# Optimization experiments

Hardware: AMD Instinct MI355X
Metric: run time of the kernel (lower is better)

Reference implementation:

```python
import jax, jax.numpy as jnp
import numpy as np

B, H, W, D = 16, 64, 64, 512

def setup_inputs() -> dict:
    key = jax.random.key(0)
    k1, k2, k3, k4, k5, k6 = jax.random.split(key, 6)
    x = jax.random.normal(k1, (B, H, W, D), dtype=jnp.float32)
    attentionXFull = jax.random.normal(k2, (B, H, W, W), dtype=jnp.float32)
    attentionYFull = jax.random.normal(k3, (B, W, H, H), dtype=jnp.float32)
    valueFull = jax.random.normal(k4, (B, H, W, D), dtype=jnp.float32)
    # Learned scalar Gaussian params: shift initialized positive, bias negative
    shift = jnp.abs(jax.random.normal(k5, (1,), dtype=jnp.float32))
    bias = -jnp.abs(jax.random.normal(k6, (1,), dtype=jnp.float32))
    return {"x": x, "attentionXFull": attentionXFull, "attentionYFull": attentionYFull,
            "valueFull": valueFull, "shift": shift, "bias": bias}

def reference(x, attentionXFull, attentionYFull, valueFull, shift, bias):
    # valueFull: [B,H,W,D]; attentionXFull: [B,H,W,W] (last axis = row positions h)
    # attentionYFull: [B,W,H,H] (indexed [b,c,r,w], last axis = col positions w)
    Bv, Hd, Wd, Dd = valueFull.shape
    cw = jnp.arange(Wd, dtype=valueFull.dtype)
    # disX[c,h] = -(shift*(h-c)^2 + bias)
    disX = -(shift[0] * (cw[None, :] - cw[:, None]) ** 2 + bias[0])  # [W,W]
    aX = jax.nn.sigmoid(disX[None, None, :, :] + attentionXFull)     # [B,H,W,W]
    outX = jnp.einsum('brch,brhd->brcd', aX, valueFull)              # row attention
    rh = jnp.arange(Hd, dtype=valueFull.dtype)
    # disY[r,w] = -(shift*(w-r)^2 + bias)
    disY = -(shift[0] * (rh[None, :] - rh[:, None]) ** 2 + bias[0])  # [H,H]
    aY = jax.nn.sigmoid(disY[None, None, :, :] + attentionYFull)     # [B,W,H,H] as [b,c,r,w]
    outY = jnp.einsum('bcrw,bwcd->brcd', aY, valueFull)              # column attention
    return outX + outY
```

## Files before the change

### kernel.cpp

```cpp
#include <hip/hip_runtime.h>
#include <stdint.h>


typedef __attribute__((ext_vector_type(8))) __bf16 bf16x8;
typedef __attribute__((ext_vector_type(8))) short short8;
typedef __attribute__((ext_vector_type(4))) float f32x4;
typedef __attribute__((ext_vector_type(4))) unsigned int uint4v;
typedef __attribute__((ext_vector_type(4))) unsigned short u16x4;

union U8 { short8 s; bf16x8 b; unsigned short u[8]; uint4v q; };

__device__ __forceinline__ unsigned short f2bf(float f) {
    union { float f; unsigned int i; } v; v.f = f;
    return (unsigned short)((v.i + 0x7fffu + ((v.i >> 16) & 1u)) >> 16);
}
__device__ __forceinline__ float fsigmoid(float x) {
    float e = __builtin_amdgcn_exp2f(-1.44269504f * x);
    return __builtin_amdgcn_rcpf(1.0f + e);
}
__device__ __forceinline__ unsigned short f2h(float f) {
    union { _Float16 h; unsigned short u; } v; v.h = (_Float16)f; return v.u;
}
__device__ __forceinline__ float h2f(unsigned short u) {
    union { _Float16 h; unsigned short us; } v; v.us = u; return (float)v.h;
}

__device__ __forceinline__ void sig16(const float* __restrict__ in,
                                      unsigned short* __restrict__ outp,
                                      int l0, int sec, float shift, float bias) {
    f32x4 v[4];
#pragma unroll
    for (int j = 0; j < 4; ++j) v[j] = *(const f32x4*)(in + 4 * j);
    U8 r0, r1;
#pragma unroll
    for (int e = 0; e < 16; ++e) {
        float dd = (float)(l0 + e - sec);
        float dis = -(shift * dd * dd + bias);
        unsigned short us = f2bf(fsigmoid(dis + v[e >> 2][e & 3]));
        if (e < 8) r0.u[e] = us; else r1.u[e - 8] = us;
    }
    *(uint4v*)(outp) = r0.q;
    *(uint4v*)(outp + 8) = r1.q;
}

__global__ __launch_bounds__(256)
void prep_sig(const float* __restrict__ attX, const float* __restrict__ attY,
              unsigned short* __restrict__ aX, unsigned short* __restrict__ aY,
              const float* __restrict__ shiftp, const float* __restrict__ biasp) {
    const float shift = shiftp[0];
    const float bias  = biasp[0];
    const size_t base = ((size_t)blockIdx.x * 256 + threadIdx.x) * 16;
    const int sec = (int)((base >> 6) & 63);
    const int l0  = (int)(base & 63);
    sig16(attX + base, aX + base, l0, sec, shift, bias);
    sig16(attY + base, aY + base, l0, sec, shift, bias);
}

__global__ __launch_bounds__(256, 4)
void gauss_fused2(const unsigned short* __restrict__ aX,
                  const unsigned short* __restrict__ aY,
                  const float* __restrict__ V,
                  float* __restrict__ out) {
    __shared__ unsigned short park[4 * 4224];

    const int p   = blockIdx.x;
    const int xcd = p & 7;
    const int s   = p >> 3;
    const int b   = xcd + ((s >> 6) << 3);
    const int rem = s & 63;
    const int dt  = rem >> 2;
    const int rt  = rem & 3;

    const int t    = threadIdx.x;
    const int lane = t & 63;
    const int ct   = t >> 6;
    const int l15  = lane & 15, quad = lane >> 4;

    unsigned short* pk = &park[ct * 4224];

    const size_t vbase = (size_t)b * 2097152;
    const unsigned short* aXb = aX + (size_t)b * 262144;
    const unsigned short* aYb = aY + (size_t)b * 262144;

    for (int dc = 0; dc < 2; ++dc) {
        const int dcol = dt * 32 + dc * 16 + l15;

        const float* vxw = V + vbase + (size_t)(rt * 16) * 32768 + dcol;
        const unsigned short* axw = aXb + ((size_t)(rt * 16) * 64 + ct * 16 + l15) * 64 + quad * 8;
#pragma unroll 2
        for (int rr = 0; rr < 16; ++rr) {
            const float* vp = vxw + (size_t)rr * 32768;
            const unsigned short* ap = axw + (size_t)rr * 4096;
            f32x4 acc = (f32x4)0.0f;
#pragma unroll
            for (int ks = 0; ks < 2; ++ks) {
                const int h0 = ks * 32 + quad * 8;
                float vf[8];
#pragma unroll
                for (int j = 0; j < 8; ++j) vf[j] = vp[(h0 + j) * 512];
                U8 a; a.q = *(const uint4v*)(ap + ks * 32);
                U8 bb;
#pragma unroll
                for (int j = 0; j < 8; ++j) bb.u[j] = f2bf(vf[j]);
                acc = __builtin_amdgcn_mfma_f32_16x16x32_bf16(a.b, bb.b, acc, 0, 0, 0);
            }
            u16x4 w;
#pragma unroll
            for (int g = 0; g < 4; ++g) w[g] = f2h(acc[g]);
            *(u16x4*)&pk[l15 * 264 + rr * 16 + quad * 4] = w;
        }

        const float* vyw = V + vbase + (size_t)(ct * 16) * 512 + dcol;
        const unsigned short* ayw = aYb + ((size_t)(ct * 16) * 64 + rt * 16 + l15) * 64 + quad * 8;
        float* ow = out + vbase + (size_t)(rt * 16 + quad * 4) * 32768
                  + (size_t)(ct * 16) * 512 + dcol;
#pragma unroll 2
        for (int cc = 0; cc < 16; ++cc) {
            const float* vp = vyw + (size_t)cc * 512;
            const unsigned short* ap = ayw + (size_t)cc * 4096;
            f32x4 acc = (f32x4)0.0f;
#pragma unroll
            for (int ks = 0; ks < 2; ++ks) {
                const int w0 = ks * 32 + quad * 8;
                float vf[8];
#pragma unroll
                for (int j = 0; j < 8; ++j) vf[j] = vp[(size_t)(w0 + j) * 32768];
                U8 a; a.q = *(const uint4v*)(ap + ks * 32);
                U8 bb;
#pragma unroll
                for (int j = 0; j < 8; ++j) bb.u[j] = f2bf(vf[j]);
                acc = __builtin_amdgcn_mfma_f32_16x16x32_bf16(a.b, bb.b, acc, 0, 0, 0);
            }
#pragma unroll
            for (int g = 0; g < 4; ++g) {
                float xv = h2f(pk[l15 * 264 + (quad * 4 + g) * 16 + cc]);
                ow[(size_t)g * 32768 + (size_t)cc * 512] = acc[g] + xv;
            }
        }
    }
}

template <int S_I, int S_K, bool ACCUM>
__global__ __launch_bounds__(256)
void gauss_gemm(const float* __restrict__ att,
                const float* __restrict__ V,
                float* __restrict__ out,
                const float* __restrict__ shiftp,
                const float* __restrict__ biasp) {
    __shared__ unsigned short S[4096];
    __shared__ unsigned short VT[128 * 66];

    const int bid    = blockIdx.x;
    const int dq     = bid & 3;
    const int i      = (bid >> 2) & 63;
    const int b      = bid >> 8;
    const int t      = threadIdx.x;
    const int dstart = dq * 128;

    const float shift = shiftp[0];
    const float bias  = biasp[0];
    const size_t base = (size_t)b * 2097152 + (size_t)i * S_I;

    const float* ab = att + (size_t)(b * 64 + i) * 4096;
#pragma unroll
    for (int chunk = 0; chunk < 2; ++chunk) {
        int flat = t + chunk * 256;
        int qd = flat >> 6, m = flat & 63;
        const float* ap = ab + m * 64 + qd * 8;
        f32x4 av0 = *(const f32x4*)(ap);
        f32x4 av1 = *(const f32x4*)(ap + 4);
        U8 res;
#pragma unroll
        for (int j = 0; j < 8; ++j) {
            float a    = (j < 4) ? av0[j & 3] : av1[j & 3];
            float diff = (float)(qd * 8 + j - m);
            float dis  = -(shift * diff * diff + bias);
            res.u[j]   = f2bf(fsigmoid(dis + a));
        }
        *(short8*)(&S[flat * 8]) = res.s;
    }
    {
        const float* vb = V + base + dstart;
        const int d4 = t & 31;
        const int h0 = t >> 5;
#pragma unroll
        for (int it = 0; it < 8; ++it) {
            const int h = h0 + it * 8;
            f32x4 v = *(const f32x4*)(vb + (size_t)h * S_K + 4 * d4);
#pragma unroll
            for (int u = 0; u < 4; ++u)
                VT[(4 * d4 + u) * 66 + h] = f2bf(v[u]);
        }
    }
    __syncthreads();

    const int lane = t & 63, wid = t >> 6;
    const int l15 = lane & 15, quad = lane >> 4;

    f32x4 acc[4][2];
#pragma unroll
    for (int mt = 0; mt < 4; ++mt)
#pragma unroll
        for (int nt = 0; nt < 2; ++nt) acc[mt][nt] = (f32x4)0.0f;

#pragma unroll
    for (int ks = 0; ks < 2; ++ks) {
        bf16x8 af[4];
#pragma unroll
        for (int mt = 0; mt < 4; ++mt) {
            U8 a;
            a.s = *(const short8*)(&S[((ks * 4 + quad) * 64 + mt * 16 + l15) * 8]);
            af[mt] = a.b;
        }
        const int h = ks * 32 + quad * 8;
#pragma unroll
        for (int nt = 0; nt < 2; ++nt) {
            const int dloc = wid * 32 + nt * 16 + l15;
            const unsigned short* vp = &VT[dloc * 66 + h];
            U8 bvec;
            uint4v qv;
#pragma unroll
            for (int u = 0; u < 4; ++u) qv[u] = *(const unsigned int*)(vp + 2 * u);
            bvec.q = qv;
#pragma unroll
            for (int mt = 0; mt < 4; ++mt)
                acc[mt][nt] = __builtin_amdgcn_mfma_f32_16x16x32_bf16(
                    af[mt], bvec.b, acc[mt][nt], 0, 0, 0);
        }
    }

    float* ob = out + base + dstart;
#pragma unroll
    for (int mt = 0; mt < 4; ++mt)
#pragma unroll
        for (int nt = 0; nt < 2; ++nt)
#pragma unroll
            for (int reg = 0; reg < 4; ++reg) {
                int m = mt * 16 + quad * 4 + reg;
                int d = wid * 32 + nt * 16 + l15;
                size_t off = (size_t)m * S_K + d;
                float v = acc[mt][nt][reg];
                if (ACCUM) v += ob[off];
                ob[off] = v;
            }
}

extern "C" void kernel_launch(void* const* d_in, const int* in_sizes, int n_in,
                              void* d_out, int out_size, void* d_ws, size_t ws_size,
                              hipStream_t stream) {
    const float* attX = (const float*)d_in[1];
    const float* attY = (const float*)d_in[2];
    const float* V    = (const float*)d_in[3];
    const float* shp  = (const float*)d_in[4];
    const float* bip  = (const float*)d_in[5];
    float* out = (float*)d_out;

    const size_t A_ELEMS = 4194304;
    const size_t NEED = 2 * A_ELEMS * sizeof(unsigned short);

    if (ws_size >= NEED) {
        unsigned short* aXw = (unsigned short*)d_ws;
        unsigned short* aYw = aXw + A_ELEMS;
        prep_sig<<<dim3(1024), dim3(256), 0, stream>>>(attX, attY, aXw, aYw, shp, bip);
        gauss_fused2<<<dim3(1024), dim3(256), 0, stream>>>(aXw, aYw, V, out);
    } else {
        dim3 blk(256);
        dim3 grid(16 * 64 * 4);
        gauss_gemm<32768, 512, false><<<grid, blk, 0, stream>>>(attX, V, out, shp, bip);
        gauss_gemm<512, 32768, true><<<grid, blk, 0, stream>>>(attY, V, out, shp, bip);
    }
}
```

Before: 465.6 us.

## Process two adjacent D columns per lane with float2 loads and dual MFMAs

Each lane now loads float2 pairs of V along D and drives two MFMA accumulators, so one pass covers the 32-wide D tile instead of looping over two 16-wide halves. The parked row-attention results are stored interleaved per column pair in a larger shared buffer, and the final outputs are written as float2. The aim is to widen global accesses and reuse the A fragment loads across two MFMAs. In exchange, LDS use and register pressure roughly double, and launch bounds drop to 2 blocks per CU, which cuts occupancy.

```diff
diff --git a/kernel.cpp b/kernel.cpp
--- a/kernel.cpp
+++ b/kernel.cpp
@@ -4,6 +4,7 @@
 
 typedef __attribute__((ext_vector_type(8))) __bf16 bf16x8;
 typedef __attribute__((ext_vector_type(8))) short short8;
+typedef __attribute__((ext_vector_type(2))) float f32x2;
 typedef __attribute__((ext_vector_type(4))) float f32x4;
 typedef __attribute__((ext_vector_type(4))) unsigned int uint4v;
 typedef __attribute__((ext_vector_type(4))) unsigned short u16x4;
@@ -23,6 +24,10 @@
 }
 __device__ __forceinline__ float h2f(unsigned short u) {
     union { _Float16 h; unsigned short us; } v; v.us = u; return (float)v.h;
+}
+
+__device__ __forceinline__ int park_off(int d2, int r, int c, int e) {
+    return d2 * 580 + r * 36 + c * 2 + e;
 }
 
 __device__ __forceinline__ void sig16(const float* __restrict__ in,
@@ -56,85 +61,90 @@
     sig16(attY + base, aY + base, l0, sec, shift, bias);
 }
 
-__global__ __launch_bounds__(256, 4)
-void gauss_fused2(const unsigned short* __restrict__ aX,
+__global__ __launch_bounds__(256, 2)
+void gauss_fused3(const unsigned short* __restrict__ aX,
                   const unsigned short* __restrict__ aY,
                   const float* __restrict__ V,
                   float* __restrict__ out) {
-    __shared__ unsigned short park[4 * 4224];
+    __shared__ unsigned short park[4 * 9280];
 
     const int p   = blockIdx.x;
     const int xcd = p & 7;
     const int s   = p >> 3;
     const int b   = xcd + ((s >> 6) << 3);
-    const int rem = s & 63;
-    const int dt  = rem >> 2;
-    const int rt  = rem & 3;
+    const int dt  = (s >> 2) & 15;
+    const int rt  = s & 3;
 
     const int t    = threadIdx.x;
     const int lane = t & 63;
     const int ct   = t >> 6;
     const int l15  = lane & 15, quad = lane >> 4;
-
-    unsigned short* pk = &park[ct * 4224];
+    const int d0   = dt * 32;
+
+    unsigned short* mypark = &park[ct * 9280];
 
     const size_t vbase = (size_t)b * 2097152;
     const unsigned short* aXb = aX + (size_t)b * 262144;
     const unsigned short* aYb = aY + (size_t)b * 262144;
 
-    for (int dc = 0; dc < 2; ++dc) {
-        const int dcol = dt * 32 + dc * 16 + l15;
-
-        const float* vxw = V + vbase + (size_t)(rt * 16) * 32768 + dcol;
+    {
+        const float* vxw = V + vbase + (size_t)(rt * 16) * 32768 + d0 + 2 * l15;
         const unsigned short* axw = aXb + ((size_t)(rt * 16) * 64 + ct * 16 + l15) * 64 + quad * 8;
 #pragma unroll 2
         for (int rr = 0; rr < 16; ++rr) {
             const float* vp = vxw + (size_t)rr * 32768;
             const unsigned short* ap = axw + (size_t)rr * 4096;
-            f32x4 acc = (f32x4)0.0f;
+            f32x4 acc0 = (f32x4)0.0f, acc1 = (f32x4)0.0f;
 #pragma unroll
             for (int ks = 0; ks < 2; ++ks) {
                 const int h0 = ks * 32 + quad * 8;
-                float vf[8];
-#pragma unroll
-                for (int j = 0; j < 8; ++j) vf[j] = vp[(h0 + j) * 512];
+                f32x2 vf[8];
+#pragma unroll
+                for (int j = 0; j < 8; ++j) vf[j] = *(const f32x2*)(vp + (h0 + j) * 512);
                 U8 a; a.q = *(const uint4v*)(ap + ks * 32);
-                U8 bb;
-#pragma unroll
-                for (int j = 0; j < 8; ++j) bb.u[j] = f2bf(vf[j]);
-                acc = __builtin_amdgcn_mfma_f32_16x16x32_bf16(a.b, bb.b, acc, 0, 0, 0);
-            }
-            u16x4 w;
-#pragma unroll
-            for (int g = 0; g < 4; ++g) w[g] = f2h(acc[g]);
-            *(u16x4*)&pk[l15 * 264 + rr * 16 + quad * 4] = w;
-        }
-
-        const float* vyw = V + vbase + (size_t)(ct * 16) * 512 + dcol;
+                U8 b0, b1;
+#pragma unroll
+                for (int j = 0; j < 8; ++j) { b0.u[j] = f2bf(vf[j][0]); b1.u[j] = f2bf(vf[j][1]); }
+                acc0 = __builtin_amdgcn_mfma_f32_16x16x32_bf16(a.b, b0.b, acc0, 0, 0, 0);
+                acc1 = __builtin_amdgcn_mfma_f32_16x16x32_bf16(a.b, b1.b, acc1, 0, 0, 0);
+            }
+            U8 pk;
+#pragma unroll
+            for (int g = 0; g < 4; ++g) { pk.u[g * 2] = f2h(acc0[g]); pk.u[g * 2 + 1] = f2h(acc1[g]); }
+            *(uint4v*)&mypark[park_off(l15, rr, quad * 4, 0)] = pk.q;
+        }
+    }
+
+    {
+        const float* vyw = V + vbase + (size_t)(ct * 16) * 512 + d0 + 2 * l15;
         const unsigned short* ayw = aYb + ((size_t)(ct * 16) * 64 + rt * 16 + l15) * 64 + quad * 8;
         float* ow = out + vbase + (size_t)(rt * 16 + quad * 4) * 32768
-                  + (size_t)(ct * 16) * 512 + dcol;
+                  + (size_t)(ct * 16) * 512 + d0 + 2 * l15;
 #pragma unroll 2
         for (int cc = 0; cc < 16; ++cc) {
             const float* vp = vyw + (size_t)cc * 512;
             const unsigned short* ap = ayw + (size_t)cc * 4096;
-            f32x4 acc = (f32x4)0.0f;
+            f32x4 acc0 = (f32x4)0.0f, acc1 = (f32x4)0.0f;
 #pragma unroll
             for (int ks = 0; ks < 2; ++ks) {
                 const int w0 = ks * 32 + quad * 8;
-                float vf[8];
-#pragma unroll
-                for (int j = 0; j < 8; ++j) vf[j] = vp[(size_t)(w0 + j) * 32768];
+                f32x2 vf[8];
+#pragma unroll
+                for (int j = 0; j < 8; ++j) vf[j] = *(const f32x2*)(vp + (size_t)(w0 + j) * 32768);
                 U8 a; a.q = *(const uint4v*)(ap + ks * 32);
-                U8 bb;
-#pragma unroll
-                for (int j = 0; j < 8; ++j) bb.u[j] = f2bf(vf[j]);
-                acc = __builtin_amdgcn_mfma_f32_16x16x32_bf16(a.b, bb.b, acc, 0, 0, 0);
+                U8 b0, b1;
+#pragma unroll
+                for (int j = 0; j < 8; ++j) { b0.u[j] = f2bf(vf[j][0]); b1.u[j] = f2bf(vf[j][1]); }
+                acc0 = __builtin_amdgcn_mfma_f32_16x16x32_bf16(a.b, b0.b, acc0, 0, 0, 0);
+                acc1 = __builtin_amdgcn_mfma_f32_16x16x32_bf16(a.b, b1.b, acc1, 0, 0, 0);
             }
 #pragma unroll
             for (int g = 0; g < 4; ++g) {
-                float xv = h2f(pk[l15 * 264 + (quad * 4 + g) * 16 + cc]);
-                ow[(size_t)g * 32768 + (size_t)cc * 512] = acc[g] + xv;
+                const unsigned short* pp = &mypark[park_off(l15, quad * 4 + g, cc, 0)];
+                f32x2 res;
+                res[0] = acc0[g] + h2f(pp[0]);
+                res[1] = acc1[g] + h2f(pp[1]);
+                *(f32x2*)(ow + (size_t)g * 32768 + (size_t)cc * 512) = res;
             }
         }
     }
@@ -262,7 +272,7 @@
         unsigned short* aXw = (unsigned short*)d_ws;
         unsigned short* aYw = aXw + A_ELEMS;
         prep_sig<<<dim3(1024), dim3(256), 0, stream>>>(attX, attY, aXw, aYw, shp, bip);
-        gauss_fused2<<<dim3(1024), dim3(256), 0, stream>>>(aXw, aYw, V, out);
+        gauss_fused3<<<dim3(1024), dim3(256), 0, stream>>>(aXw, aYw, V, out);
     } else {
         dim3 blk(256);
         dim3 grid(16 * 64 * 4);
```

New measurement: 379.1 us. 18.6% less time.
